# Kernel tuning notes

Hardware: AMD Instinct MI355X
Metric: run time of the kernel (lower is better)

## Reference

```python
import jax, jax.numpy as jnp
import numpy as np

N = 4096  # num_dev == num_task (required by elementwise msg computation)
D = 64    # embed_dim


def setup_inputs() -> dict:
    key = jax.random.key(0)
    ks = jax.random.split(key, 10)
    return {
        "embed": jax.random.normal(ks[0], (2 * N, D), jnp.float32),
        "adj_collab": jnp.zeros((N, N), jnp.float32),   # only .shape[0] is used
        "adj_interact": jnp.zeros((N, N), jnp.float32),  # unused in forward body
        "adj_similar": jnp.zeros((N, N), jnp.float32),   # unused in forward body
        "collab_score": jax.random.normal(ks[1], (N, N), jnp.float32),
        "interact_score": jax.random.normal(ks[2], (N, N), jnp.float32),
        "similar_score": jax.random.normal(ks[3], (N, N), jnp.float32),
        "deg_dev": jax.random.uniform(ks[4], (N,), jnp.float32, 1.0, 100.0),
        "deg_task": jax.random.uniform(ks[5], (N,), jnp.float32, 1.0, 100.0),
        "W1": jax.random.normal(ks[6], (D, D), jnp.float32) / np.sqrt(D).astype(np.float32),
        "b1": jnp.zeros((D,), jnp.float32),
        "W2": jax.random.normal(ks[7], (D, D), jnp.float32) / np.sqrt(D).astype(np.float32),
        "b2": jnp.zeros((D,), jnp.float32),
        "W3": jax.random.normal(ks[8], (D, D), jnp.float32) / np.sqrt(D).astype(np.float32),
        "b3": jnp.zeros((D,), jnp.float32),
    }


def _linear(x, W, b):
    # torch nn.Linear: x @ W.T + b
    return x @ W.T + b


def _calc_attention(src, dst, rel_score, src_deg, dst_deg):
    # msg = dst + src*dst ; per-row dot <src, msg> ; degree + sqrt(d) scaling ; softmax
    msg = dst + src * dst                      # [N, D]
    dot = jnp.sum(src * msg, axis=-1)          # [N]
    scale = dot / (jnp.sqrt(src_deg * dst_deg + 1e-8) * jnp.sqrt(jnp.float32(src.shape[-1])))
    att = jax.nn.softmax(rel_score * scale, axis=-1)  # [N, N] (scale broadcasts over columns)
    return att, msg


def reference(embed, adj_collab, adj_interact, adj_similar,
              collab_score, interact_score, similar_score,
              deg_dev, deg_task, W1, b1, W2, b2, W3, b3):
    num_dev = adj_collab.shape[0]
    dev = embed[:num_dev]       # [N, D]
    task = embed[num_dev:]      # [N, D]

    collab_att, collab_msg = _calc_attention(dev, dev, collab_score, deg_dev, deg_dev)
    collab_prop = collab_att @ _linear(collab_msg, W1, b1)

    interact_att, interact_msg = _calc_attention(dev, task, interact_score, deg_dev, deg_task)
    interact_prop = interact_att @ _linear(interact_msg, W2, b2)

    dev_prop = jax.nn.leaky_relu(_linear(dev + collab_prop + interact_prop, W3, b3), 0.2)

    similar_att, _similar_msg = _calc_attention(task, task, similar_score, deg_task, deg_task)
    similar_prop = similar_att @ _linear(task, W3, b3)  # note: original uses W3(task_embed), not the msg
    task_prop = jax.nn.leaky_relu(_linear(task + similar_prop, W3, b3), 0.2)

    # dropout omitted (eval mode / identity)
    return jnp.concatenate([dev_prop, task_prop], axis=0)
```

## Files before the change

kernel.cpp:

```cpp
#include <hip/hip_runtime.h>
#include <math.h>

#define N 4096
#define D 64
#define ROWS 128
#define NSLICE 8
#define JLEN 512
#define CH 32
#define NCHUNK 16
#define SH 44.0f

#define S_OFF   0
#define MT_OFF  32768
#define E_OFF   40960
#define SCL_OFF 49152
#define LDS_BYTES 51200

typedef short bf16x8 __attribute__((ext_vector_type(8)));
typedef float f32x4  __attribute__((ext_vector_type(4)));

__device__ __forceinline__ unsigned short f2bf(float x) {
    unsigned int u = __float_as_uint(x);
    u += 0x7FFFu + ((u >> 16) & 1u);
    return (unsigned short)(u >> 16);
}
__device__ __forceinline__ float bf2f(unsigned short h) {
    return __uint_as_float(((unsigned int)h) << 16);
}

__device__ __forceinline__ void gld16(const void* g, void* l) {
    __builtin_amdgcn_global_load_lds(
        (const __attribute__((address_space(1))) void*)g,
        (__attribute__((address_space(3))) void*)l,
        16, 0, 0);
}

__device__ __forceinline__ void lds_barrier() {
    asm volatile("s_waitcnt lgkmcnt(0)" ::: "memory");
    __builtin_amdgcn_s_barrier();
    asm volatile("" ::: "memory");
}
__device__ __forceinline__ void plain_barrier() {
    asm volatile("" ::: "memory");
    __builtin_amdgcn_s_barrier();
    asm volatile("" ::: "memory");
}

__global__ __launch_bounds__(256) void prep_kernel(
    const float* __restrict__ embed,
    const float* __restrict__ degd, const float* __restrict__ degt,
    const float* __restrict__ W1, const float* __restrict__ b1,
    const float* __restrict__ W2, const float* __restrict__ b2,
    const float* __restrict__ W3, const float* __restrict__ b3,
    float* __restrict__ scale, unsigned short* __restrict__ Mt)
{
    const int rel = blockIdx.y;
    const float* W  = (rel == 0) ? W1 : (rel == 1 ? W2 : W3);
    const float* bb = (rel == 0) ? b1 : (rel == 1 ? b2 : b3);
    __shared__ float Wl[D][D + 1];
    __shared__ float xr[4][D];
    __shared__ unsigned short ot[4][D];
    const int tid = threadIdx.x;
    for (int idx = tid; idx < D * D; idx += 256)
        Wl[idx >> 6][idx & 63] = W[idx];
    const int w = tid >> 6, d = tid & 63;
    const int i0 = blockIdx.x * 4;
    const int i = i0 + w;

    float msg, term, xsrc, dga, dgb;
    if (rel == 0) {
        float s = embed[(size_t)i * D + d];
        msg = s + s * s; term = s * msg; xsrc = msg;
        dga = degd[i]; dgb = degd[i];
    } else if (rel == 1) {
        float s = embed[(size_t)i * D + d];
        float t = embed[(size_t)(N + i) * D + d];
        msg = t + s * t; term = s * msg; xsrc = msg;
        dga = degd[i]; dgb = degt[i];
    } else {
        float t = embed[(size_t)(N + i) * D + d];
        msg = t + t * t; term = t * msg; xsrc = t;
        dga = degt[i]; dgb = degt[i];
    }
    float dot = term;
    #pragma unroll
    for (int mm = 1; mm < 64; mm <<= 1) dot += __shfl_xor(dot, mm);
    if (d == 0)
        scale[rel * N + i] = dot / (sqrtf(dga * dgb + 1e-8f) * 8.0f);

    xr[w][d] = xsrc;
    __syncthreads();
    float o = bb[d];
    #pragma unroll 8
    for (int k = 0; k < D; ++k) o += xr[w][k] * Wl[d][k];
    ot[w][d] = f2bf(o);
    __syncthreads();
    if (tid < 64) {
        union { unsigned short h[4]; uint2 v; } t;
        t.h[0] = ot[0][tid]; t.h[1] = ot[1][tid];
        t.h[2] = ot[2][tid]; t.h[3] = ot[3][tid];
        *(uint2*)&Mt[((size_t)rel * D + tid) * N + i0] = t.v;
    }
}

__global__ __launch_bounds__(256, 3) void attn_kernel(
    const float* __restrict__ S0, const float* __restrict__ S1, const float* __restrict__ S2,
    const float* __restrict__ scale, const unsigned short* __restrict__ Mt,
    unsigned short* __restrict__ Up, float* __restrict__ lp)
{
    __shared__ __align__(16) char LDS[LDS_BYTES];
    const int rg = blockIdx.x, rel = blockIdx.y, sl = blockIdx.z;
    const float* S = (rel == 0) ? S0 : (rel == 1 ? S1 : S2);
    const unsigned short* Mtr = Mt + (size_t)rel * D * N;
    const int tid = threadIdx.x;
    const int lane = tid & 63, wave = tid >> 6;
    const int row = tid >> 1, q = tid & 1;
    const int j0 = sl * JLEN;

    const int sr8 = lane >> 3, sslot = lane & 7;
    const int sgx = (sslot ^ sr8) * 4;
    const float* spb = S + (size_t)(rg * ROWS + wave * 32 + sr8) * N + j0 + sgx;
    const unsigned short* mtp = Mtr + (size_t)lane * N + j0 + wave * 8;
    char* sldsw = LDS + S_OFF + wave * 4096;
    char* mldsw = LDS + MT_OFF + wave * 1024;

#define ISSUE_S(cc, bb) do {                                                   \
        gld16(spb + (size_t)0 * 8 * N + (cc) * CH, sldsw + (bb) * 16384);      \
        gld16(spb + (size_t)1 * 8 * N + (cc) * CH, sldsw + (bb) * 16384 + 1024); \
        gld16(spb + (size_t)2 * 8 * N + (cc) * CH, sldsw + (bb) * 16384 + 2048); \
        gld16(spb + (size_t)3 * 8 * N + (cc) * CH, sldsw + (bb) * 16384 + 3072); \
    } while (0)
#define ISSUE_M(cc, bb) gld16(mtp + (cc) * CH, mldsw + (bb) * 4096)

    for (int k = tid; k < JLEN; k += 256)
        *(float*)(LDS + SCL_OFF + k * 4) = scale[rel * N + j0 + k];
    asm volatile("" ::: "memory");
    ISSUE_S(0, 0);
    ISSUE_M(0, 0);
    ISSUE_S(1, 1);
    lds_barrier();

    const int lrow = lane & 15;
    const int lk   = lane >> 4;
    float l = 0.f;
    f32x4 acc[2][4];
    #pragma unroll
    for (int t = 0; t < 2; ++t)
        #pragma unroll
        for (int ct = 0; ct < 4; ++ct) {
            acc[t][ct][0] = 0.f; acc[t][ct][1] = 0.f;
            acc[t][ct][2] = 0.f; acc[t][ct][3] = 0.f;
        }

    #pragma unroll
    for (int c = 0; c < NCHUNK; ++c) {
        if (c < NCHUNK - 1) asm volatile("s_waitcnt vmcnt(4)" ::: "memory");
        else                asm volatile("s_waitcnt vmcnt(0)" ::: "memory");
        plain_barrier();

        if (c + 1 < NCHUNK) ISSUE_M(c + 1, (c + 1) & 1);

        {
            const char* sb = LDS + S_OFF + (c & 1) * 16384 + row * 128;
            const int r7 = row & 7;
            const f32x4 s0 = *(const f32x4*)(sb + (((q * 4 + 0) ^ r7) << 4));
            const f32x4 s1 = *(const f32x4*)(sb + (((q * 4 + 1) ^ r7) << 4));
            const f32x4 s2 = *(const f32x4*)(sb + (((q * 4 + 2) ^ r7) << 4));
            const f32x4 s3 = *(const f32x4*)(sb + (((q * 4 + 3) ^ r7) << 4));
            const char* cb = LDS + SCL_OFF + c * 128 + q * 64;
            const f32x4 c0 = *(const f32x4*)(cb);
            const f32x4 c1 = *(const f32x4*)(cb + 16);
            const f32x4 c2 = *(const f32x4*)(cb + 32);
            const f32x4 c3 = *(const f32x4*)(cb + 48);
            float e[16];
            #pragma unroll
            for (int u = 0; u < 4; ++u) {
                e[u]      = __expf(fmaf(s0[u], c0[u], -SH));
                e[4 + u]  = __expf(fmaf(s1[u], c1[u], -SH));
                e[8 + u]  = __expf(fmaf(s2[u], c2[u], -SH));
                e[12 + u] = __expf(fmaf(s3[u], c3[u], -SH));
            }
            #pragma unroll
            for (int k = 0; k < 16; ++k) l += e[k];
            union { unsigned short h[8]; uint4 v; } p0, p1;
            #pragma unroll
            for (int k = 0; k < 8; ++k) { p0.h[k] = f2bf(e[k]); p1.h[k] = f2bf(e[8 + k]); }
            const int kgA = 2 * q, kgB = 2 * q + 1;
            *(uint4*)(LDS + E_OFF + kgA * 2048 + ((row ^ (2 * kgA)) << 4)) = p0.v;
            *(uint4*)(LDS + E_OFF + kgB * 2048 + ((row ^ (2 * kgB)) << 4)) = p1.v;
        }

        lds_barrier();

        if (c + 2 < NCHUNK) ISSUE_S(c + 2, c & 1);

        {
            const char* mb = LDS + MT_OFF + (c & 1) * 4096 + lk * 1024;
            const int ra0 = wave * 32 + lrow, ra1 = wave * 32 + 16 + lrow;
            const bf16x8 a0 = *(const bf16x8*)(
                LDS + E_OFF + lk * 2048 + ((ra0 ^ (2 * lk)) << 4));
            const bf16x8 a1 = *(const bf16x8*)(
                LDS + E_OFF + lk * 2048 + ((ra1 ^ (2 * lk)) << 4));
            #pragma unroll
            for (int ct = 0; ct < 4; ++ct) {
                const bf16x8 b = *(const bf16x8*)(mb + ((ct * 16 + lrow) << 4));
                acc[0][ct] = __builtin_amdgcn_mfma_f32_16x16x32_bf16(a0, b, acc[0][ct], 0, 0, 0);
                acc[1][ct] = __builtin_amdgcn_mfma_f32_16x16x32_bf16(a1, b, acc[1][ct], 0, 0, 0);
            }
        }
    }
#undef ISSUE_S
#undef ISSUE_M

    unsigned short* R = (unsigned short*)LDS;
    #pragma unroll
    for (int t = 0; t < 2; ++t)
        #pragma unroll
        for (int ct = 0; ct < 4; ++ct)
            #pragma unroll
            for (int r = 0; r < 4; ++r) {
                const int ri = wave * 32 + t * 16 + lk * 4 + r;
                R[ri * 64 + ct * 16 + lrow] = f2bf(acc[t][ct][r]);
            }
    lds_barrier();
    const size_t pbase = (size_t)((rel * 32 + rg) * NSLICE + sl);
    unsigned short* up = Up + pbase * 8192;
    {
        const uint4* src = (const uint4*)R;
        uint4*       dst = (uint4*)up;
        dst[tid]       = src[tid];
        dst[256 + tid] = src[256 + tid];
        dst[512 + tid] = src[512 + tid];
        dst[768 + tid] = src[768 + tid];
    }
    l += __shfl_xor(l, 1);
    if (q == 0) lp[pbase * ROWS + row] = l;
}

__device__ __forceinline__ float combine_row(
    const unsigned short* __restrict__ Up, const float* __restrict__ lp,
    int rel, int i, int d)
{
    const int rt = i >> 7, r = i & 127;
    const int base = (rel * 32 + rt) * NSLICE;
    float lt = 0.f, u = 0.f;
    #pragma unroll
    for (int p = 0; p < NSLICE; ++p) {
        lt += lp[(base + p) * ROWS + r];
        u  += bf2f(Up[(size_t)(base + p) * 8192 + r * 64 + d]);
    }
    return u / lt;
}

__global__ __launch_bounds__(256) void final_kernel(
    const float* __restrict__ embed,
    const unsigned short* __restrict__ Up, const float* __restrict__ lp,
    const float* __restrict__ W3, const float* __restrict__ b3,
    float* __restrict__ out)
{
    __shared__ float Wl[D][D + 1];
    __shared__ float xs[4][D];
    const int tid = threadIdx.x;
    for (int idx = tid; idx < D * D; idx += 256)
        Wl[idx >> 6][idx & 63] = W3[idx];
    const int w = tid >> 6, d = tid & 63;
    const int g = blockIdx.x * 4 + w;

    float x = embed[(size_t)g * D + d];
    if (g < N) {
        x += combine_row(Up, lp, 0, g, d);
        x += combine_row(Up, lp, 1, g, d);
    } else {
        x += combine_row(Up, lp, 2, g - N, d);
    }
    xs[w][d] = x;
    __syncthreads();
    float o = b3[d];
    #pragma unroll 8
    for (int k = 0; k < D; ++k) o += xs[w][k] * Wl[d][k];
    o = (o > 0.f) ? o : 0.2f * o;
    out[(size_t)g * D + d] = o;
}

extern "C" void kernel_launch(void* const* d_in, const int* in_sizes, int n_in,
                              void* d_out, int out_size, void* d_ws, size_t ws_size,
                              hipStream_t stream)
{
    const float* embed = (const float*)d_in[0];
    const float* Sc   = (const float*)d_in[4];
    const float* Si   = (const float*)d_in[5];
    const float* Ss   = (const float*)d_in[6];
    const float* degd = (const float*)d_in[7];
    const float* degt = (const float*)d_in[8];
    const float* W1 = (const float*)d_in[9];
    const float* b1 = (const float*)d_in[10];
    const float* W2 = (const float*)d_in[11];
    const float* b2 = (const float*)d_in[12];
    const float* W3 = (const float*)d_in[13];
    const float* b3 = (const float*)d_in[14];
    float* out = (float*)d_out;

    float* ws    = (float*)d_ws;
    float* scale = ws;
    float* lp    = ws + 12288;
    unsigned short* Mt = (unsigned short*)(lp + 98304);
    unsigned short* Up = Mt + 786432;

    prep_kernel<<<dim3(N / 4, 3), 256, 0, stream>>>(
        embed, degd, degt, W1, b1, W2, b2, W3, b3, scale, Mt);
    attn_kernel<<<dim3(N / ROWS, 3, NSLICE), 256, 0, stream>>>(
        Sc, Si, Ss, scale, Mt, Up, lp);
    final_kernel<<<dim3(2 * N / 4), 256, 0, stream>>>(
        embed, Up, lp, W3, b3, out);
}
```

Before: 58.98 us.

## Make attention waves self-contained, drop mid-chunk barrier, remap blocks per XCD

Result: no change. 58.40 us (-1.0%).

```diff
diff --git a/kernel.cpp b/kernel.cpp
--- a/kernel.cpp
+++ b/kernel.cpp
@@ -37,11 +37,6 @@
 
 __device__ __forceinline__ void lds_barrier() {
     asm volatile("s_waitcnt lgkmcnt(0)" ::: "memory");
-    __builtin_amdgcn_s_barrier();
-    asm volatile("" ::: "memory");
-}
-__device__ __forceinline__ void plain_barrier() {
-    asm volatile("" ::: "memory");
     __builtin_amdgcn_s_barrier();
     asm volatile("" ::: "memory");
 }
@@ -109,39 +104,45 @@
     unsigned short* __restrict__ Up, float* __restrict__ lp)
 {
     __shared__ __align__(16) char LDS[LDS_BYTES];
-    const int rg = blockIdx.x, rel = blockIdx.y, sl = blockIdx.z;
+    const int bid = blockIdx.x;
+    const int xcd = bid & 7, idx = bid >> 3;
+    const int pair = xcd * 3 + (idx >> 5);
+    const int rg = idx & 31;
+    const int rel = pair >> 3, sl = pair & 7;
+
     const float* S = (rel == 0) ? S0 : (rel == 1 ? S1 : S2);
     const unsigned short* Mtr = Mt + (size_t)rel * D * N;
     const int tid = threadIdx.x;
     const int lane = tid & 63, wave = tid >> 6;
-    const int row = tid >> 1, q = tid & 1;
     const int j0 = sl * JLEN;
 
     const int sr8 = lane >> 3, sslot = lane & 7;
     const int sgx = (sslot ^ sr8) * 4;
     const float* spb = S + (size_t)(rg * ROWS + wave * 32 + sr8) * N + j0 + sgx;
     const unsigned short* mtp = Mtr + (size_t)lane * N + j0 + wave * 8;
-    char* sldsw = LDS + S_OFF + wave * 4096;
+    char* sldsw = LDS + S_OFF + wave * 8192;
     char* mldsw = LDS + MT_OFF + wave * 1024;
 
-#define ISSUE_S(cc, bb) do {                                                   \
-        gld16(spb + (size_t)0 * 8 * N + (cc) * CH, sldsw + (bb) * 16384);      \
-        gld16(spb + (size_t)1 * 8 * N + (cc) * CH, sldsw + (bb) * 16384 + 1024); \
-        gld16(spb + (size_t)2 * 8 * N + (cc) * CH, sldsw + (bb) * 16384 + 2048); \
-        gld16(spb + (size_t)3 * 8 * N + (cc) * CH, sldsw + (bb) * 16384 + 3072); \
+#define ISSUE_S(cc, bb) do {                                                     \
+        gld16(spb + (size_t)0 * 8 * N + (cc) * CH, sldsw + (bb) * 4096);         \
+        gld16(spb + (size_t)1 * 8 * N + (cc) * CH, sldsw + (bb) * 4096 + 1024);  \
+        gld16(spb + (size_t)2 * 8 * N + (cc) * CH, sldsw + (bb) * 4096 + 2048);  \
+        gld16(spb + (size_t)3 * 8 * N + (cc) * CH, sldsw + (bb) * 4096 + 3072);  \
     } while (0)
 #define ISSUE_M(cc, bb) gld16(mtp + (cc) * CH, mldsw + (bb) * 4096)
 
-    for (int k = tid; k < JLEN; k += 256)
-        *(float*)(LDS + SCL_OFF + k * 4) = scale[rel * N + j0 + k];
-    asm volatile("" ::: "memory");
     ISSUE_S(0, 0);
     ISSUE_M(0, 0);
     ISSUE_S(1, 1);
+    for (int k = tid; k < JLEN; k += 256)
+        *(float*)(LDS + SCL_OFF + k * 4) = scale[rel * N + j0 + k];
     lds_barrier();
 
-    const int lrow = lane & 15;
-    const int lk   = lane >> 4;
+    const int r = lane >> 1, q = lane & 1;
+    const int r7 = r & 7;
+    const int lrow = lane & 15, lk = lane >> 4;
+    char* Ew = LDS + E_OFF + wave * 2048;
+
     float l = 0.f;
     f32x4 acc[2][4];
     #pragma unroll
@@ -156,13 +157,12 @@
     for (int c = 0; c < NCHUNK; ++c) {
         if (c < NCHUNK - 1) asm volatile("s_waitcnt vmcnt(4)" ::: "memory");
         else                asm volatile("s_waitcnt vmcnt(0)" ::: "memory");
-        plain_barrier();
+        lds_barrier();
 
         if (c + 1 < NCHUNK) ISSUE_M(c + 1, (c + 1) & 1);
 
         {
-            const char* sb = LDS + S_OFF + (c & 1) * 16384 + row * 128;
-            const int r7 = row & 7;
+            const char* sb = sldsw + (c & 1) * 4096 + r * 128;
             const f32x4 s0 = *(const f32x4*)(sb + (((q * 4 + 0) ^ r7) << 4));
             const f32x4 s1 = *(const f32x4*)(sb + (((q * 4 + 1) ^ r7) << 4));
             const f32x4 s2 = *(const f32x4*)(sb + (((q * 4 + 2) ^ r7) << 4));
@@ -185,22 +185,18 @@
             union { unsigned short h[8]; uint4 v; } p0, p1;
             #pragma unroll
             for (int k = 0; k < 8; ++k) { p0.h[k] = f2bf(e[k]); p1.h[k] = f2bf(e[8 + k]); }
-            const int kgA = 2 * q, kgB = 2 * q + 1;
-            *(uint4*)(LDS + E_OFF + kgA * 2048 + ((row ^ (2 * kgA)) << 4)) = p0.v;
-            *(uint4*)(LDS + E_OFF + kgB * 2048 + ((row ^ (2 * kgB)) << 4)) = p1.v;
+            *(uint4*)(Ew + (2 * q)     * 512 + (r << 4)) = p0.v;
+            *(uint4*)(Ew + (2 * q + 1) * 512 + (r << 4)) = p1.v;
         }
 
-        lds_barrier();
-
+        asm volatile("s_waitcnt lgkmcnt(0)" ::: "memory");
         if (c + 2 < NCHUNK) ISSUE_S(c + 2, c & 1);
 
+        __builtin_amdgcn_s_setprio(1);
         {
             const char* mb = LDS + MT_OFF + (c & 1) * 4096 + lk * 1024;
-            const int ra0 = wave * 32 + lrow, ra1 = wave * 32 + 16 + lrow;
-            const bf16x8 a0 = *(const bf16x8*)(
-                LDS + E_OFF + lk * 2048 + ((ra0 ^ (2 * lk)) << 4));
-            const bf16x8 a1 = *(const bf16x8*)(
-                LDS + E_OFF + lk * 2048 + ((ra1 ^ (2 * lk)) << 4));
+            const bf16x8 a0 = *(const bf16x8*)(Ew + lk * 512 + (lrow << 4));
+            const bf16x8 a1 = *(const bf16x8*)(Ew + lk * 512 + ((16 + lrow) << 4));
             #pragma unroll
             for (int ct = 0; ct < 4; ++ct) {
                 const bf16x8 b = *(const bf16x8*)(mb + ((ct * 16 + lrow) << 4));
@@ -208,33 +204,31 @@
                 acc[1][ct] = __builtin_amdgcn_mfma_f32_16x16x32_bf16(a1, b, acc[1][ct], 0, 0, 0);
             }
         }
+        __builtin_amdgcn_s_setprio(0);
     }
 #undef ISSUE_S
 #undef ISSUE_M
 
-    unsigned short* R = (unsigned short*)LDS;
+    unsigned short* Rw = (unsigned short*)(sldsw);
     #pragma unroll
     for (int t = 0; t < 2; ++t)
         #pragma unroll
         for (int ct = 0; ct < 4; ++ct)
             #pragma unroll
-            for (int r = 0; r < 4; ++r) {
-                const int ri = wave * 32 + t * 16 + lk * 4 + r;
-                R[ri * 64 + ct * 16 + lrow] = f2bf(acc[t][ct][r]);
+            for (int rr = 0; rr < 4; ++rr) {
+                const int ri = t * 16 + lk * 4 + rr;
+                Rw[ri * 64 + ct * 16 + lrow] = f2bf(acc[t][ct][rr]);
             }
-    lds_barrier();
+    asm volatile("s_waitcnt lgkmcnt(0)" ::: "memory");
     const size_t pbase = (size_t)((rel * 32 + rg) * NSLICE + sl);
-    unsigned short* up = Up + pbase * 8192;
+    char* up = (char*)(Up + pbase * 8192) + wave * 4096;
     {
-        const uint4* src = (const uint4*)R;
-        uint4*       dst = (uint4*)up;
-        dst[tid]       = src[tid];
-        dst[256 + tid] = src[256 + tid];
-        dst[512 + tid] = src[512 + tid];
-        dst[768 + tid] = src[768 + tid];
+        const uint4* src = (const uint4*)((const char*)Rw + lane * 64);
+        uint4*       dst = (uint4*)(up + lane * 64);
+        dst[0] = src[0]; dst[1] = src[1]; dst[2] = src[2]; dst[3] = src[3];
     }
     l += __shfl_xor(l, 1);
-    if (q == 0) lp[pbase * ROWS + row] = l;
+    if (q == 0) lp[pbase * ROWS + wave * 32 + r] = l;
 }
 
 __device__ __forceinline__ float combine_row(
@@ -308,7 +302,7 @@
 
     prep_kernel<<<dim3(N / 4, 3), 256, 0, stream>>>(
         embed, degd, degt, W1, b1, W2, b2, W3, b3, scale, Mt);
-    attn_kernel<<<dim3(N / ROWS, 3, NSLICE), 256, 0, stream>>>(
+    attn_kernel<<<dim3((N / ROWS) * 3 * NSLICE), 256, 0, stream>>>(
         Sc, Si, Ss, scale, Mt, Up, lp);
     final_kernel<<<dim3(2 * N / 4), 256, 0, stream>>>(
         embed, Up, lp, W3, b3, out);
```
